# Performance work log

Measured on AMD Instinct MI355X. Metric: run time of the kernel, lower is better.

## Reference

```python
import jax, jax.numpy as jnp
import numpy as np

# Config (mirrors CorrLayerDownsample(J=3, L=8, A=1, A_prime=1, M=256, N=256,
# num_channels=1, shift_mode='samec', mask_angles=4)). With samec + 1 channel,
# every pair is 'shifted' (mask index 1) and groups (j1,j2) are contiguous in
# the global moment order, so concatenation reproduces results_storage order.
J, L, A, M, N, NB = 3, 8, 1, 256, 256, 2
MASK_ANGLES = 4
RADII = (1, 2)  # dyadic shift radii (assumed form of create_masks_shift)

def _mask_positions():
    # shift mask 1: origin plus shifts along mask_angles directions at dyadic radii
    pos = {(0, 0)}
    for k in range(MASK_ANGLES):
        th = np.pi * k / MASK_ANGLES
        for r in RADII:
            pos.add((int(round(r * np.cos(th))), int(round(r * np.sin(th)))))
    return sorted(pos)

def _union_flat_idx(h, w):
    # row-major flat indices of the union shift mask at resolution (h, w),
    # matching torch boolean-mask indexing order (mask_downsample + mask_idx_map_1)
    return np.array(sorted(((dx % h) * w + (dy % w)) for dx, dy in _mask_positions()), dtype=np.int64)

UNION_IDX = [_union_flat_idx(M >> j, N >> j) for j in range(J)]
NSHIFT = len(UNION_IDX[0])

# per-(j1,j2) channel gather indices: la = A*L*c + A*l + a = l (A=1, c=0)
# loop order in compute_idx: l1 outer, l2 inner
LA1 = np.repeat(np.arange(L), L)
LA2 = np.tile(np.arange(L), L)

def _spectral_pad(xh, Mn, Nn):
    # zero-pad Fourier representation to (Mn, Nn) -- spectral upsampling
    m, n = xh.shape[-2], xh.shape[-1]
    if (m, n) == (Mn, Nn):
        return xh
    xs = jnp.fft.fftshift(xh, axes=(-2, -1))
    ph, pw = (Mn - m) // 2, (Nn - n) // 2
    pad = [(0, 0)] * (xh.ndim - 2) + [(ph, ph), (pw, pw)]
    xp = jnp.pad(xs, pad)
    return jnp.fft.ifftshift(xp, axes=(-2, -1)) * ((Mn * Nn) / (m * n))

def _forward(xpsi_0, xpsi_1, xpsi_2):
    xs = [xpsi_0, xpsi_1, xpsi_2]
    hats = [jnp.fft.fft2(x.astype(jnp.complex64)) for x in xs]  # [nb, C, h_j, w_j]
    la1 = jnp.asarray(LA1)
    la2 = jnp.asarray(LA2)
    outs = []
    for j1 in range(J):
        h, w = M >> j1, N >> j1
        uidx = jnp.asarray(UNION_IDX[j1])
        h1 = hats[j1][:, la1]  # [nb, P=L*L, h, w]
        for j2 in range(j1, J):
            h2 = hats[j2][:, la2]
            if j2 > j1:
                h2 = _spectral_pad(h2, h, w)  # upsample coarser scale to scale j1
            corr = jnp.fft.ifft2(h1 * jnp.conj(h2)).real  # cross-correlation map
            flat = corr.reshape(corr.shape[0], corr.shape[1], h * w)
            outs.append(flat[:, :, uidx])  # masked downsample: keep shift positions
    return jnp.concatenate(outs, axis=1)  # [nb, total_pairs, NSHIFT]

def setup_inputs():
    key = jax.random.key(0)
    ks = jax.random.split(key, 3)
    return {
        "xpsi_0": jax.random.normal(ks[0], (NB, A * L, M, N), dtype=jnp.float32),
        "xpsi_1": jax.random.normal(ks[1], (NB, A * L, M // 2, N // 2), dtype=jnp.float32),
        "xpsi_2": jax.random.normal(ks[2], (NB, A * L, M // 4, N // 4), dtype=jnp.float32),
    }

def reference(xpsi_0, xpsi_1, xpsi_2):
    return _forward(xpsi_0, xpsi_1, xpsi_2)
```

## Files before the change

### kernel.cpp

```cpp
#include <hip/hip_runtime.h>

#define PI_D 3.14159265358979323846
#define PI_F 3.14159265358979323846f


__device__ inline float rtab_val(int n, int m2, int t) {
  if (t == 0) return 1.0f;
  double th = PI_D * (double)t / (double)n;
  double v = sin(th * (double)(m2 - 1)) / sin(th) + cos(th * (double)m2);
  return (float)(v / (double)m2);
}

template <int NR>
__device__ __forceinline__ void phaseA256(const float* __restrict__ vch,
                                          const float* __restrict__ sRl,
                                          float* __restrict__ sh,
                                          const int (&rls)[NR], int mxg, int s,
                                          int n2, float inv, float Pv, float a,
                                          int per, int cid) {
  int bj[NR];
#pragma unroll
  for (int j = 0; j < NR; ++j) bj[j] = (mxg - 2 + rls[j]) & 255;
  float4 acc[NR];
#pragma unroll
  for (int j = 0; j < NR; ++j) acc[j] = make_float4(0.f, 0.f, 0.f, 0.f);
  const float4* vp = (const float4*)vch + cid;
  float4 cur[8], nxt[8];
#pragma unroll
  for (int k = 0; k < 8; ++k) cur[k] = vp[(size_t)k * 64];
  for (int nx = 0; nx < n2; nx += 8) {
    if (nx + 8 < n2) {
#pragma unroll
      for (int k = 0; k < 8; ++k) nxt[k] = vp[(size_t)(nx + 8 + k) * 64];
    }
#pragma unroll
    for (int k = 0; k < 8; ++k) {
      int ss = s * (nx + k);
#pragma unroll
      for (int j = 0; j < NR; ++j) {
        float rv = sRl[(bj[j] - ss) & 255];
        acc[j].x += rv * cur[k].x;
        acc[j].y += rv * cur[k].y;
        acc[j].z += rv * cur[k].z;
        acc[j].w += rv * cur[k].w;
      }
    }
#pragma unroll
    for (int k = 0; k < 8; ++k) cur[k] = nxt[k];
  }
  float smy[4];
#pragma unroll
  for (int j = 0; j < 4; ++j)
    smy[j] = sinf(a * (float)((4 * cid + j) & (per - 1)));
#pragma unroll
  for (int j = 0; j < NR; ++j) {
    float q = inv * sinf(a * (float)(bj[j] & (per - 1))) * Pv;
    float4 o = acc[j];
    o.x -= q * smy[0];
    o.y -= q * smy[1];
    o.z -= q * smy[2];
    o.w -= q * smy[3];
    *(float4*)&sh[rls[j] * 256 + 4 * cid] = o;
  }
}

template <int NR>
__device__ __forceinline__ void phaseA128(const float* __restrict__ vch,
                                          const float* __restrict__ sRl,
                                          float* __restrict__ sh,
                                          const int (&rls)[NR], int mxg, int n2,
                                          float inv, float Pv, int cid) {
  int bj[NR];
#pragma unroll
  for (int j = 0; j < NR; ++j) bj[j] = (mxg - 2 + rls[j]) & 127;
  float2 acc[NR];
#pragma unroll
  for (int j = 0; j < NR; ++j) acc[j] = make_float2(0.f, 0.f);
  const float2* vp = (const float2*)vch + cid;
  float2 cur[8], nxt[8];
#pragma unroll
  for (int k = 0; k < 8; ++k) cur[k] = vp[(size_t)k * 64];
  for (int nx = 0; nx < n2; nx += 8) {
    if (nx + 8 < n2) {
#pragma unroll
      for (int k = 0; k < 8; ++k) nxt[k] = vp[(size_t)(nx + 8 + k) * 64];
    }
#pragma unroll
    for (int k = 0; k < 8; ++k) {
      int ss = 2 * (nx + k);
#pragma unroll
      for (int j = 0; j < NR; ++j) {
        float rv = sRl[(bj[j] - ss) & 127];
        acc[j].x += rv * cur[k].x;
        acc[j].y += rv * cur[k].y;
      }
    }
#pragma unroll
    for (int k = 0; k < 8; ++k) cur[k] = nxt[k];
  }
  const float a = PI_F * 0.5f;
  float smy0 = sinf(a * (float)((2 * cid) & 3));
  float smy1 = sinf(a * (float)((2 * cid + 1) & 3));
#pragma unroll
  for (int j = 0; j < NR; ++j) {
    float q = inv * sinf(a * (float)(bj[j] & 3)) * Pv;
    float2 o = acc[j];
    o.x -= q * smy0;
    o.y -= q * smy1;
    *(float2*)&sh[rls[j] * 128 + 2 * cid] = o;
  }
}

__global__ __launch_bounds__(256) void k_front(
    const float* __restrict__ X0, const float* __restrict__ X1,
    const float* __restrict__ X2, float* __restrict__ P1p,
    float* __restrict__ P2p, float* __restrict__ V01, float* __restrict__ V02,
    float* __restrict__ V12, float* __restrict__ T01, float* __restrict__ T02,
    float* __restrict__ T12, float* __restrict__ out) {
  __shared__ float fsm[3840];
  int bid = blockIdx.x;
  int t = threadIdx.x;
  if (bid < 192) {
    const float* X; float* P; int lg, nsp, idx0;
    if (bid < 128) { X = X1; P = P1p; lg = 7; nsp = 8; idx0 = bid; }
    else           { X = X2; P = P2p; lg = 6; nsp = 4; idx0 = bid - 128; }
    int ch = idx0 / nsp, split = idx0 % nsp;
    int n = 1 << lg;
    int total = n * n;
    int chunk = total / nsp;
    int b0 = split * chunk;
    const float* x = X + (size_t)ch * total + b0;
    float s = 0.f;
    for (int i = t; i < chunk; i += 256) {
      int idx = b0 + i;
      float v = x[i];
      s += (((idx >> lg) ^ idx) & 1) ? -v : v;
    }
#pragma unroll
    for (int off = 32; off > 0; off >>= 1) s += __shfl_down(s, off, 64);
    __shared__ float red[4];
    if ((t & 63) == 0) red[t >> 6] = s;
    __syncthreads();
    if (t == 0) P[ch * nsp + split] = red[0] + red[1] + red[2] + red[3];
    return;
  }
  if (bid < 320) {
    int idx = bid - 192;
    int ch = idx >> 3, nxg = (idx & 7) * 16;
    float* Rl = fsm;
    float* Xs = fsm + 256;
    for (int i = t; i < 256; i += 256) Rl[i] = rtab_val(256, 128, i);
    const float4* xch4 =
        (const float4*)(X1 + (size_t)ch * 16384 + (size_t)nxg * 128);
    for (int i = t; i < 512; i += 256) ((float4*)Xs)[i] = xch4[i];
    __syncthreads();
    if (idx == 0)
      for (int i = t; i < 256; i += 256) T01[i] = Rl[i];
    float* vch = V01 + (size_t)ch * 128 * 256;
    for (int i = t; i < 2048; i += 256) {
      int r = i >> 7, k = i & 127;
      vch[(size_t)(nxg + r) * 256 + 2 * k] = Xs[r * 128 + k];
    }
    int cid = t & 63, wq = t >> 6;
    int m0 = 2 * cid + 1, m1 = 2 * cid + 129;
    float acc[4][2];
#pragma unroll
    for (int r = 0; r < 4; ++r) { acc[r][0] = 0.f; acc[r][1] = 0.f; }
    for (int ny = 0; ny < 128; ++ny) {
      float r0 = Rl[(m0 - 2 * ny) & 255];
      float r1 = Rl[(m1 - 2 * ny) & 255];
#pragma unroll
      for (int r = 0; r < 4; ++r) {
        float xv = Xs[(4 * wq + r) * 128 + ny];
        acc[r][0] += xv * r0;
        acc[r][1] += xv * r1;
      }
    }
#pragma unroll
    for (int r = 0; r < 4; ++r) {
      vch[(size_t)(nxg + 4 * wq + r) * 256 + m0] = acc[r][0];
      vch[(size_t)(nxg + 4 * wq + r) * 256 + m1] = acc[r][1];
    }
    return;
  }
  if (bid < 512) {
    int vbid = bid - 320;
    const float* X = X2; float* V;
    int n1, n2, s, ch, nxg, colh;
    if (vbid < 128) {
      V = V02; n1 = 256; n2 = 64; s = 4;
      ch = vbid >> 3; nxg = ((vbid >> 1) & 3) * 16; colh = vbid & 1;
    } else {
      int w = vbid - 128;
      V = V12; n1 = 128; n2 = 64; s = 2;
      ch = w >> 2; nxg = (w & 3) * 16; colh = 0;
    }
    float* Rl = fsm;
    float* Xs = fsm + 256;
    for (int i = t; i < n1; i += 256) Rl[i] = rtab_val(n1, n2, i);
    const float4* xch4 =
        (const float4*)(X + (size_t)ch * n2 * n2 + (size_t)nxg * n2);
    int nx4 = (16 * n2) >> 2;
    for (int i = t; i < nx4; i += 256) ((float4*)Xs)[i] = xch4[i];
    __syncthreads();
    if (vbid == 0)
      for (int i = t; i < 256; i += 256) T02[i] = Rl[i];
    if (vbid == 128)
      for (int i = t; i < 128; i += 256) T12[i] = Rl[i];
    int myq = (t & 63) + colh * 128;
    int nxq = t >> 6;
    int mask = n1 - 1;
    float acc[4][2];
#pragma unroll
    for (int r = 0; r < 4; ++r)
#pragma unroll
      for (int c = 0; c < 2; ++c) acc[r][c] = 0.f;
    for (int ny = 0; ny < n2; ++ny) {
      float xv[4];
#pragma unroll
      for (int r = 0; r < 4; ++r) xv[r] = Xs[(4 * nxq + r) * n2 + ny];
#pragma unroll
      for (int c = 0; c < 2; ++c) {
        float rv = Rl[(myq + 64 * c - s * ny) & mask];
#pragma unroll
        for (int r = 0; r < 4; ++r) acc[r][c] += xv[r] * rv;
      }
    }
    float* vch = V + (size_t)ch * n2 * n1;
#pragma unroll
    for (int r = 0; r < 4; ++r)
      for (int c = 0; c < 2; ++c)
        vch[(size_t)(nxg + 4 * nxq + r) * n1 + myq + 64 * c] = acc[r][c];
    return;
  }
  int lane = t & 63;
  int wv = t >> 6;
  float accC[8][7];
#pragma unroll
  for (int i = 0; i < 8; ++i)
#pragma unroll
    for (int p = 0; p < 7; ++p) accC[i][p] = 0.f;
  int w = bid - 512;
  const float* Ab; int loc, lgn1, lgc, base;
  if (w < 256)      { loc = w;       Ab = X0; lgn1 = 8; lgc = 4; base = 0;   }
  else if (w < 384) { loc = w - 256; Ab = X1; lgn1 = 7; lgc = 3; base = 192; }
  else              { loc = w - 384; Ab = X2; lgn1 = 6; lgc = 2; base = 320; }
  int n1 = 1 << lgn1;
  int mask = n1 - 1;
  int n1sq = n1 * n1;
  int chunk = loc & ((1 << lgc) - 1);
  int bl2 = loc >> lgc;
  int b = bl2 >> 3, l2 = bl2 & 7;
  const float* A1 = Ab + (size_t)(b * 8) * n1sq;
  const float* A2 = Ab + (size_t)(b * 8 + l2) * n1sq;
  int lgtpr = lgn1 - 2;
  int tpr = 1 << lgtpr;
  int rif = 256 >> lgtpr;
  int rid = t >> lgtpr;
  int cid2 = t & (tpr - 1);
  int ty = cid2 * 4;
  int tym = (ty - 4) & mask;
  for (int rr = 0; rr < 16; rr += rif) {
    int row = chunk * 16 + rr + rid;
    const float* r0 = A2 + (size_t)row * n1;
    const float* r1 = A2 + (size_t)((row - 1) & mask) * n1;
    const float* r2 = A2 + (size_t)((row - 2) & mask) * n1;
    const float* r3 = A2 + (size_t)((row + 1) & mask) * n1;
    float4 a0 = *(const float4*)(r0 + tym);
    float4 b0 = *(const float4*)(r0 + ty);
    float4 a1 = *(const float4*)(r1 + tym);
    float4 b1 = *(const float4*)(r1 + ty);
    float4 b2 = *(const float4*)(r2 + ty);
    float4 a3 = *(const float4*)(r3 + tym);
    float4 b3 = *(const float4*)(r3 + ty);
    const float* rA = A1 + (size_t)row * n1 + ty;
#pragma unroll
    for (int l1 = 0; l1 < 8; ++l1) {
      float4 xv = *(const float4*)(rA + (size_t)l1 * n1sq);
      accC[l1][0] += xv.x * b0.x + xv.y * b0.y + xv.z * b0.z + xv.w * b0.w;
      accC[l1][1] += xv.x * a0.w + xv.y * b0.x + xv.z * b0.y + xv.w * b0.z;
      accC[l1][2] += xv.x * a0.z + xv.y * a0.w + xv.z * b0.x + xv.w * b0.y;
      accC[l1][3] += xv.x * b1.x + xv.y * b1.y + xv.z * b1.z + xv.w * b1.w;
      accC[l1][4] += xv.x * a1.w + xv.y * b1.x + xv.z * b1.y + xv.w * b1.z;
      accC[l1][5] += xv.x * b2.x + xv.y * b2.y + xv.z * b2.z + xv.w * b2.w;
      accC[l1][6] += xv.x * a3.w + xv.y * b3.x + xv.z * b3.y + xv.w * b3.z;
    }
  }
  float* sh = fsm;
  float* af = &accC[0][0];
#pragma unroll
  for (int j = 0; j < 56; ++j) {
    float v = af[j];
    v += __shfl_down(v, 32, 64);
    v += __shfl_down(v, 16, 64);
    af[j] = v;
  }
  __syncthreads();
  if (lane < 16) {
    float* rowp = sh + (wv * 16 + lane) * 60;
#pragma unroll
    for (int j = 0; j < 14; ++j)
      *(float4*)&rowp[4 * j] =
          make_float4(af[4 * j], af[4 * j + 1], af[4 * j + 2], af[4 * j + 3]);
  }
  __syncthreads();
  if (t < 224) {
    int v = t >> 2, q = t & 3;
    float s2 = 0.f;
#pragma unroll
    for (int i = 0; i < 16; ++i) s2 += sh[(q * 16 + i) * 60 + v];
    s2 += __shfl_down(s2, 2, 64);
    s2 += __shfl_down(s2, 1, 64);
    if (q == 0) {
      int l1o = v / 7, p = v % 7;
      atomicAdd(&out[((size_t)b * 384 + base + l1o * 8 + l2) * 7 + p], s2);
    }
  }
}

__global__ __launch_bounds__(256) void k_main(const float* __restrict__ X0,
                                              const float* __restrict__ X1,
                                              const float* __restrict__ V01,
                                              const float* __restrict__ V02,
                                              const float* __restrict__ V12,
                                              const float* __restrict__ P1p,
                                              const float* __restrict__ P2p,
                                              const float* __restrict__ T01,
                                              const float* __restrict__ T02,
                                              const float* __restrict__ T12,
                                              float* __restrict__ out) {
  __shared__ float sRl[256];
  __shared__ float sh[4864];
  int u = blockIdx.x;
  int t = threadIdx.x;
  int lane = t & 63;
  int wv = t >> 6;

  float accC[8][7];
#pragma unroll
  for (int i = 0; i < 8; ++i)
#pragma unroll
    for (int p = 0; p < 7; ++p) accC[i][p] = 0.f;

  const float* V; const float* Pp; const float* A1b; const float* T;
  int n1, n2, s, ch, chunk, nsp, lgn1, base; float inv;
  if (u < 256) {
    V = V01; Pp = P1p; nsp = 8; A1b = X0; n1 = 256; n2 = 128; s = 2;
    inv = 1.f / 16384.f; ch = u >> 4; chunk = u & 15; lgn1 = 8; base = 64;
    T = T01;
  } else if (u < 512) {
    int w = u - 256;
    V = V02; Pp = P2p; nsp = 4; A1b = X0; n1 = 256; n2 = 64; s = 4;
    inv = 1.f / 4096.f; ch = w >> 4; chunk = w & 15; lgn1 = 8; base = 128;
    T = T02;
  } else {
    int w = u - 512;
    V = V12; Pp = P2p; nsp = 4; A1b = X1; n1 = 128; n2 = 64; s = 2;
    inv = 1.f / 4096.f; ch = w >> 3; chunk = w & 7; lgn1 = 7; base = 256;
    T = T12;
  }
  int mask = n1 - 1;
  for (int i = t; i < n1; i += 256) sRl[i] = T[i];
  __syncthreads();
  int mxg = chunk * 16;
  int b = ch >> 3, l2 = ch & 7;
  const float* vch = V + (size_t)ch * n2 * n1;
  float Pv = 0.f;
  for (int i = 0; i < nsp; ++i) Pv += Pp[ch * nsp + i];
  float a = PI_F / (float)s;
  int per = 2 * s;

  if (n1 == 256) {
    if (s == 2) {
      if (wv < 3) {
        int rls[3] = {6 * wv + 1, 6 * wv + 3, 6 * wv + 5};
        phaseA256<3>(vch, sRl, sh, rls, mxg, 2, 128, inv, Pv, a, per, lane);
      } else {
        for (int i = lane; i < 640; i += 64) {
          int rl = 2 * (i >> 6), c4 = (i & 63) * 4;
          int mx = (mxg - 2 + rl) & 255;
          *(float4*)&sh[rl * 256 + c4] =
              *(const float4*)(vch + (size_t)(mx >> 1) * 256 + c4);
        }
      }
    } else {
      if (wv == 0) {
        int rls[4] = {0, 1, 3, 4};
        phaseA256<4>(vch, sRl, sh, rls, mxg, 4, 64, inv, Pv, a, per, lane);
      } else if (wv == 1) {
        int rls[4] = {5, 7, 8, 9};
        phaseA256<4>(vch, sRl, sh, rls, mxg, 4, 64, inv, Pv, a, per, lane);
      } else if (wv == 2) {
        int rls[3] = {11, 12, 13};
        phaseA256<3>(vch, sRl, sh, rls, mxg, 4, 64, inv, Pv, a, per, lane);
      } else {
        int rls[3] = {15, 16, 17};
        phaseA256<3>(vch, sRl, sh, rls, mxg, 4, 64, inv, Pv, a, per, lane);
      }
      for (int i = t; i < 320; i += 256) {
        int rl = 2 + 4 * (i >> 6), c4 = (i & 63) * 4;
        int mx = (mxg - 2 + rl) & 255;
        *(float4*)&sh[rl * 256 + c4] =
            *(const float4*)(vch + (size_t)(mx >> 2) * 256 + c4);
      }
    }
  } else {
    if (wv < 3) {
      int rls[3] = {6 * wv + 1, 6 * wv + 3, 6 * wv + 5};
      phaseA128<3>(vch, sRl, sh, rls, mxg, 64, inv, Pv, lane);
    } else {
      for (int i = lane; i < 320; i += 64) {
        int rl = 2 * (i >> 5), c4 = (i & 31) * 4;
        int mx = (mxg - 2 + rl) & 127;
        *(float4*)&sh[rl * 128 + c4] =
            *(const float4*)(vch + (size_t)(mx >> 1) * 128 + c4);
      }
    }
  }
  __syncthreads();

  int lgtpr = lgn1 - 2;
  int tpr = 1 << lgtpr;
  int rif = 256 >> lgtpr;
  int rid = t >> lgtpr;
  int cid2 = t & (tpr - 1);
  int ty = cid2 * 4;
  int tym = (ty - 4) & mask;
  int n1sq = n1 * n1;
  const float* A1 = A1b + (size_t)(b * 8) * n1sq;
  for (int rr = 0; rr < 16; rr += rif) {
    int ri = rr + rid;
    const float* r0 = &sh[(ri + 2) * n1];
    const float* r1 = &sh[(ri + 1) * n1];
    const float* r2 = &sh[ri * n1];
    const float* r3 = &sh[(ri + 3) * n1];
    float4 a0 = *(const float4*)(r0 + tym);
    float4 b0 = *(const float4*)(r0 + ty);
    float4 a1 = *(const float4*)(r1 + tym);
    float4 b1 = *(const float4*)(r1 + ty);
    float4 b2 = *(const float4*)(r2 + ty);
    float4 a3 = *(const float4*)(r3 + tym);
    float4 b3 = *(const float4*)(r3 + ty);
    const float* rA = A1 + (size_t)(mxg + ri) * n1 + ty;
#pragma unroll
    for (int l1 = 0; l1 < 8; ++l1) {
      float4 xv = *(const float4*)(rA + (size_t)l1 * n1sq);
      accC[l1][0] += xv.x * b0.x + xv.y * b0.y + xv.z * b0.z + xv.w * b0.w;
      accC[l1][1] += xv.x * a0.w + xv.y * b0.x + xv.z * b0.y + xv.w * b0.z;
      accC[l1][2] += xv.x * a0.z + xv.y * a0.w + xv.z * b0.x + xv.w * b0.y;
      accC[l1][3] += xv.x * b1.x + xv.y * b1.y + xv.z * b1.z + xv.w * b1.w;
      accC[l1][4] += xv.x * a1.w + xv.y * b1.x + xv.z * b1.y + xv.w * b1.z;
      accC[l1][5] += xv.x * b2.x + xv.y * b2.y + xv.z * b2.z + xv.w * b2.w;
      accC[l1][6] += xv.x * a3.w + xv.y * b3.x + xv.z * b3.y + xv.w * b3.z;
    }
  }

  float* af = &accC[0][0];
#pragma unroll
  for (int j = 0; j < 56; ++j) {
    float v = af[j];
    v += __shfl_down(v, 32, 64);
    v += __shfl_down(v, 16, 64);
    af[j] = v;
  }
  __syncthreads();
  if (lane < 16) {
    float* rowp = sh + (wv * 16 + lane) * 60;
#pragma unroll
    for (int j = 0; j < 14; ++j)
      *(float4*)&rowp[4 * j] =
          make_float4(af[4 * j], af[4 * j + 1], af[4 * j + 2], af[4 * j + 3]);
  }
  __syncthreads();
  if (t < 224) {
    int v = t >> 2, q = t & 3;
    float s2 = 0.f;
#pragma unroll
    for (int i = 0; i < 16; ++i) s2 += sh[(q * 16 + i) * 60 + v];
    s2 += __shfl_down(s2, 2, 64);
    s2 += __shfl_down(s2, 1, 64);
    if (q == 0) {
      int l1o = v / 7, p = v % 7;
      atomicAdd(&out[((size_t)b * 384 + base + l1o * 8 + l2) * 7 + p], s2);
    }
  }
}

extern "C" void kernel_launch(void* const* d_in, const int* in_sizes, int n_in,
                              void* d_out, int out_size, void* d_ws, size_t ws_size,
                              hipStream_t stream) {
  const float* X0 = (const float*)d_in[0];
  const float* X1 = (const float*)d_in[1];
  const float* X2 = (const float*)d_in[2];
  float* out = (float*)d_out;
  float* ws = (float*)d_ws;

  float* V01 = ws + 2359296;
  float* V02 = ws + 2883584;
  float* V12 = ws + 3145728;
  float* P1p = ws + 3276800;
  float* P2p = ws + 3276928;
  float* T01 = ws + 3276992;
  float* T02 = ws + 3277248;
  float* T12 = ws + 3277504;

  hipMemsetAsync(d_out, 0, (size_t)out_size, stream);
  k_front<<<960, 256, 0, stream>>>(X0, X1, X2, P1p, P2p, V01, V02, V12, T01,
                                   T02, T12, out);
  k_main<<<640, 256, 0, stream>>>(X0, X1, V01, V02, V12, P1p, P2p, T01, T02,
                                  T12, out);
}
```

Measured before the change: 114.3 us.

## Stage V tiles through double-buffered shared memory and rebalance phase-A rows across waves

Phase A of k_main previously had each wave stream V rows straight from global memory into registers. In the s==2 and n1==128 cases the fourth wave only did plain row copies. Now all 256 threads cooperatively copy 8-row tiles of V into a double-buffered shared array, with the next tile prefetched into registers. Every wave then reads the tile from LDS, and the interpolated rows are redistributed so all four waves share the arithmetic. This is meant to cut redundant global loads (four waves previously each read the same V) and balance work, at the cost of an extra 16 KB of LDS and one block barrier per tile.

```diff
diff --git a/kernel.cpp b/kernel.cpp
--- a/kernel.cpp
+++ b/kernel.cpp
@@ -9,106 +9,6 @@
   double th = PI_D * (double)t / (double)n;
   double v = sin(th * (double)(m2 - 1)) / sin(th) + cos(th * (double)m2);
   return (float)(v / (double)m2);
-}
-
-template <int NR>
-__device__ __forceinline__ void phaseA256(const float* __restrict__ vch,
-                                          const float* __restrict__ sRl,
-                                          float* __restrict__ sh,
-                                          const int (&rls)[NR], int mxg, int s,
-                                          int n2, float inv, float Pv, float a,
-                                          int per, int cid) {
-  int bj[NR];
-#pragma unroll
-  for (int j = 0; j < NR; ++j) bj[j] = (mxg - 2 + rls[j]) & 255;
-  float4 acc[NR];
-#pragma unroll
-  for (int j = 0; j < NR; ++j) acc[j] = make_float4(0.f, 0.f, 0.f, 0.f);
-  const float4* vp = (const float4*)vch + cid;
-  float4 cur[8], nxt[8];
-#pragma unroll
-  for (int k = 0; k < 8; ++k) cur[k] = vp[(size_t)k * 64];
-  for (int nx = 0; nx < n2; nx += 8) {
-    if (nx + 8 < n2) {
-#pragma unroll
-      for (int k = 0; k < 8; ++k) nxt[k] = vp[(size_t)(nx + 8 + k) * 64];
-    }
-#pragma unroll
-    for (int k = 0; k < 8; ++k) {
-      int ss = s * (nx + k);
-#pragma unroll
-      for (int j = 0; j < NR; ++j) {
-        float rv = sRl[(bj[j] - ss) & 255];
-        acc[j].x += rv * cur[k].x;
-        acc[j].y += rv * cur[k].y;
-        acc[j].z += rv * cur[k].z;
-        acc[j].w += rv * cur[k].w;
-      }
-    }
-#pragma unroll
-    for (int k = 0; k < 8; ++k) cur[k] = nxt[k];
-  }
-  float smy[4];
-#pragma unroll
-  for (int j = 0; j < 4; ++j)
-    smy[j] = sinf(a * (float)((4 * cid + j) & (per - 1)));
-#pragma unroll
-  for (int j = 0; j < NR; ++j) {
-    float q = inv * sinf(a * (float)(bj[j] & (per - 1))) * Pv;
-    float4 o = acc[j];
-    o.x -= q * smy[0];
-    o.y -= q * smy[1];
-    o.z -= q * smy[2];
-    o.w -= q * smy[3];
-    *(float4*)&sh[rls[j] * 256 + 4 * cid] = o;
-  }
-}
-
-template <int NR>
-__device__ __forceinline__ void phaseA128(const float* __restrict__ vch,
-                                          const float* __restrict__ sRl,
-                                          float* __restrict__ sh,
-                                          const int (&rls)[NR], int mxg, int n2,
-                                          float inv, float Pv, int cid) {
-  int bj[NR];
-#pragma unroll
-  for (int j = 0; j < NR; ++j) bj[j] = (mxg - 2 + rls[j]) & 127;
-  float2 acc[NR];
-#pragma unroll
-  for (int j = 0; j < NR; ++j) acc[j] = make_float2(0.f, 0.f);
-  const float2* vp = (const float2*)vch + cid;
-  float2 cur[8], nxt[8];
-#pragma unroll
-  for (int k = 0; k < 8; ++k) cur[k] = vp[(size_t)k * 64];
-  for (int nx = 0; nx < n2; nx += 8) {
-    if (nx + 8 < n2) {
-#pragma unroll
-      for (int k = 0; k < 8; ++k) nxt[k] = vp[(size_t)(nx + 8 + k) * 64];
-    }
-#pragma unroll
-    for (int k = 0; k < 8; ++k) {
-      int ss = 2 * (nx + k);
-#pragma unroll
-      for (int j = 0; j < NR; ++j) {
-        float rv = sRl[(bj[j] - ss) & 127];
-        acc[j].x += rv * cur[k].x;
-        acc[j].y += rv * cur[k].y;
-      }
-    }
-#pragma unroll
-    for (int k = 0; k < 8; ++k) cur[k] = nxt[k];
-  }
-  const float a = PI_F * 0.5f;
-  float smy0 = sinf(a * (float)((2 * cid) & 3));
-  float smy1 = sinf(a * (float)((2 * cid + 1) & 3));
-#pragma unroll
-  for (int j = 0; j < NR; ++j) {
-    float q = inv * sinf(a * (float)(bj[j] & 3)) * Pv;
-    float2 o = acc[j];
-    o.x -= q * smy0;
-    o.y -= q * smy1;
-    *(float2*)&sh[rls[j] * 128 + 2 * cid] = o;
-  }
 }
 
 __global__ __launch_bounds__(256) void k_front(
@@ -331,16 +231,11 @@
                                               float* __restrict__ out) {
   __shared__ float sRl[256];
   __shared__ float sh[4864];
+  __shared__ float Vs[2][2048];
   int u = blockIdx.x;
   int t = threadIdx.x;
   int lane = t & 63;
   int wv = t >> 6;
-
-  float accC[8][7];
-#pragma unroll
-  for (int i = 0; i < 8; ++i)
-#pragma unroll
-    for (int p = 0; p < 7; ++p) accC[i][p] = 0.f;
 
   const float* V; const float* Pp; const float* A1b; const float* T;
   int n1, n2, s, ch, chunk, nsp, lgn1, base; float inv;
@@ -361,7 +256,6 @@
   }
   int mask = n1 - 1;
   for (int i = t; i < n1; i += 256) sRl[i] = T[i];
-  __syncthreads();
   int mxg = chunk * 16;
   int b = ch >> 3, l2 = ch & 7;
   const float* vch = V + (size_t)ch * n2 * n1;
@@ -372,31 +266,13 @@
 
   if (n1 == 256) {
     if (s == 2) {
-      if (wv < 3) {
-        int rls[3] = {6 * wv + 1, 6 * wv + 3, 6 * wv + 5};
-        phaseA256<3>(vch, sRl, sh, rls, mxg, 2, 128, inv, Pv, a, per, lane);
-      } else {
-        for (int i = lane; i < 640; i += 64) {
-          int rl = 2 * (i >> 6), c4 = (i & 63) * 4;
-          int mx = (mxg - 2 + rl) & 255;
-          *(float4*)&sh[rl * 256 + c4] =
-              *(const float4*)(vch + (size_t)(mx >> 1) * 256 + c4);
-        }
+      for (int i = t; i < 640; i += 256) {
+        int rl = 2 * (i >> 6), c4 = (i & 63) * 4;
+        int mx = (mxg - 2 + rl) & 255;
+        *(float4*)&sh[rl * 256 + c4] =
+            *(const float4*)(vch + (size_t)(mx >> 1) * 256 + c4);
       }
     } else {
-      if (wv == 0) {
-        int rls[4] = {0, 1, 3, 4};
-        phaseA256<4>(vch, sRl, sh, rls, mxg, 4, 64, inv, Pv, a, per, lane);
-      } else if (wv == 1) {
-        int rls[4] = {5, 7, 8, 9};
-        phaseA256<4>(vch, sRl, sh, rls, mxg, 4, 64, inv, Pv, a, per, lane);
-      } else if (wv == 2) {
-        int rls[3] = {11, 12, 13};
-        phaseA256<3>(vch, sRl, sh, rls, mxg, 4, 64, inv, Pv, a, per, lane);
-      } else {
-        int rls[3] = {15, 16, 17};
-        phaseA256<3>(vch, sRl, sh, rls, mxg, 4, 64, inv, Pv, a, per, lane);
-      }
       for (int i = t; i < 320; i += 256) {
         int rl = 2 + 4 * (i >> 6), c4 = (i & 63) * 4;
         int mx = (mxg - 2 + rl) & 255;
@@ -405,20 +281,130 @@
       }
     }
   } else {
-    if (wv < 3) {
-      int rls[3] = {6 * wv + 1, 6 * wv + 3, 6 * wv + 5};
-      phaseA128<3>(vch, sRl, sh, rls, mxg, 64, inv, Pv, lane);
-    } else {
-      for (int i = lane; i < 320; i += 64) {
-        int rl = 2 * (i >> 5), c4 = (i & 31) * 4;
-        int mx = (mxg - 2 + rl) & 127;
-        *(float4*)&sh[rl * 128 + c4] =
-            *(const float4*)(vch + (size_t)(mx >> 1) * 128 + c4);
-      }
-    }
+    for (int i = t; i < 320; i += 256) {
+      int rl = 2 * (i >> 5), c4 = (i & 31) * 4;
+      int mx = (mxg - 2 + rl) & 127;
+      *(float4*)&sh[rl * 128 + c4] =
+          *(const float4*)(vch + (size_t)(mx >> 1) * 128 + c4);
+    }
+  }
+
+  int nr, rls[4];
+  if (s == 2) {
+    if (wv == 0)      { nr = 3; rls[0] = 1;  rls[1] = 3;  rls[2] = 5;  rls[3] = 1; }
+    else if (wv == 1) { nr = 2; rls[0] = 7;  rls[1] = 9;  rls[2] = 7;  rls[3] = 7; }
+    else if (wv == 2) { nr = 2; rls[0] = 11; rls[1] = 13; rls[2] = 11; rls[3] = 11; }
+    else              { nr = 2; rls[0] = 15; rls[1] = 17; rls[2] = 15; rls[3] = 15; }
+  } else {
+    if (wv == 0)      { nr = 4; rls[0] = 0;  rls[1] = 1;  rls[2] = 3;  rls[3] = 4; }
+    else if (wv == 1) { nr = 4; rls[0] = 5;  rls[1] = 7;  rls[2] = 8;  rls[3] = 9; }
+    else if (wv == 2) { nr = 3; rls[0] = 11; rls[1] = 12; rls[2] = 13; rls[3] = 11; }
+    else              { nr = 3; rls[0] = 15; rls[1] = 16; rls[2] = 17; rls[3] = 15; }
+  }
+  int bj[4];
+#pragma unroll
+  for (int j = 0; j < 4; ++j) bj[j] = (mxg - 2 + rls[j]) & mask;
+
+  const float4* vp4 = (const float4*)vch;
+  if (n1 == 256) {
+    int ntl = n2 >> 3;
+    for (int i = t; i < 512; i += 256) ((float4*)Vs[0])[i] = vp4[i];
+    __syncthreads();
+    float4 acc[4];
+#pragma unroll
+    for (int j = 0; j < 4; ++j) acc[j] = make_float4(0.f, 0.f, 0.f, 0.f);
+    for (int tl = 0; tl < ntl; ++tl) {
+      float4 stg0, stg1;
+      bool has = (tl + 1 < ntl);
+      if (has) {
+        stg0 = vp4[(size_t)(tl + 1) * 512 + t];
+        stg1 = vp4[(size_t)(tl + 1) * 512 + 256 + t];
+      }
+      const float* Vc = Vs[tl & 1];
+      int tb = tl * 8;
+#pragma unroll
+      for (int kk = 0; kk < 8; ++kk) {
+        float4 vv = *(const float4*)&Vc[kk * 256 + 4 * lane];
+        int ss = s * (tb + kk);
+#pragma unroll
+        for (int j = 0; j < 4; ++j)
+          if (j < nr) {
+            float rv = sRl[(bj[j] - ss) & 255];
+            acc[j].x += rv * vv.x;
+            acc[j].y += rv * vv.y;
+            acc[j].z += rv * vv.z;
+            acc[j].w += rv * vv.w;
+          }
+      }
+      if (has) {
+        float4* d = (float4*)Vs[(tl & 1) ^ 1];
+        d[t] = stg0;
+        d[256 + t] = stg1;
+      }
+      __syncthreads();
+    }
+    float smy[4];
+#pragma unroll
+    for (int j = 0; j < 4; ++j)
+      smy[j] = sinf(a * (float)((4 * lane + j) & (per - 1)));
+#pragma unroll
+    for (int j = 0; j < 4; ++j)
+      if (j < nr) {
+        float q = inv * sinf(a * (float)(bj[j] & (per - 1))) * Pv;
+        float4 o = acc[j];
+        o.x -= q * smy[0];
+        o.y -= q * smy[1];
+        o.z -= q * smy[2];
+        o.w -= q * smy[3];
+        *(float4*)&sh[rls[j] * 256 + 4 * lane] = o;
+      }
+  } else {
+    for (int i = t; i < 256; i += 256) ((float4*)Vs[0])[i] = vp4[i];
+    __syncthreads();
+    float2 acc[4];
+#pragma unroll
+    for (int j = 0; j < 4; ++j) acc[j] = make_float2(0.f, 0.f);
+    for (int tl = 0; tl < 8; ++tl) {
+      float4 stg0;
+      bool has = (tl + 1 < 8);
+      if (has) stg0 = vp4[(size_t)(tl + 1) * 256 + t];
+      const float* Vc = Vs[tl & 1];
+      int tb = tl * 8;
+#pragma unroll
+      for (int kk = 0; kk < 8; ++kk) {
+        float2 vv = *(const float2*)&Vc[kk * 128 + 2 * lane];
+        int ss = 2 * (tb + kk);
+#pragma unroll
+        for (int j = 0; j < 4; ++j)
+          if (j < nr) {
+            float rv = sRl[(bj[j] - ss) & 127];
+            acc[j].x += rv * vv.x;
+            acc[j].y += rv * vv.y;
+          }
+      }
+      if (has) ((float4*)Vs[(tl & 1) ^ 1])[t] = stg0;
+      __syncthreads();
+    }
+    const float a2 = PI_F * 0.5f;
+    float smy0 = sinf(a2 * (float)((2 * lane) & 3));
+    float smy1 = sinf(a2 * (float)((2 * lane + 1) & 3));
+#pragma unroll
+    for (int j = 0; j < 4; ++j)
+      if (j < nr) {
+        float q = inv * sinf(a2 * (float)(bj[j] & 3)) * Pv;
+        float2 o = acc[j];
+        o.x -= q * smy0;
+        o.y -= q * smy1;
+        *(float2*)&sh[rls[j] * 128 + 2 * lane] = o;
+      }
   }
   __syncthreads();
 
+  float accC[8][7];
+#pragma unroll
+  for (int i = 0; i < 8; ++i)
+#pragma unroll
+    for (int p = 0; p < 7; ++p) accC[i][p] = 0.f;
   int lgtpr = lgn1 - 2;
   int tpr = 1 << lgtpr;
   int rif = 256 >> lgtpr;
```

New measurement: 96.27 us. -15.8%, faster.
